# Kernel tuning notes

Hardware: AMD Instinct MI355X
Metric: run time of the kernel (lower is better)

Reference implementation:

```python
import jax, jax.numpy as jnp
import numpy as np

LN_EPS = 1e-5

def _reduce(t, ln_gamma, ln_beta, w_red, b_red):
    # LayerNorm(dim) then Linear(dim -> 16)
    mu = jnp.mean(t, axis=-1, keepdims=True)
    var = jnp.mean((t - mu) ** 2, axis=-1, keepdims=True)
    t = (t - mu) / jnp.sqrt(var + LN_EPS) * ln_gamma + ln_beta
    return t @ w_red + b_red  # [b, s, 16]

def setup_inputs() -> dict:
    key = jax.random.key(0)
    ks = jax.random.split(key, 4)
    b, m, n, dim, pair_dim = 1, 512, 512, 384, 128
    x = jax.random.normal(ks[0], (b, m, dim), dtype=jnp.float32)
    y = jax.random.normal(ks[1], (b, n, dim), dtype=jnp.float32)
    w_red = jax.random.normal(ks[2], (dim, 16), dtype=jnp.float32) / np.sqrt(dim)
    b_red = jnp.zeros((16,), dtype=jnp.float32)
    w_out = jax.random.normal(ks[3], (16 * 16, pair_dim), dtype=jnp.float32) / 16.0
    b_out = jnp.zeros((pair_dim,), dtype=jnp.float32)
    ln_gamma = jnp.ones((dim,), dtype=jnp.float32)
    ln_beta = jnp.zeros((dim,), dtype=jnp.float32)
    return {"x": x, "y": y, "ln_gamma": ln_gamma, "ln_beta": ln_beta,
            "w_red": w_red, "b_red": b_red, "w_out": w_out, "b_out": b_out}

def reference(x, y, ln_gamma, ln_beta, w_red, b_red, w_out, b_out):
    xr = _reduce(x, ln_gamma, ln_beta, w_red, b_red)  # [b, m, 16]
    yr = _reduce(y, ln_gamma, ln_beta, w_red, b_red)  # [b, n, 16]
    # outer product: [b, m, n, 16, 16]
    outer = jnp.einsum('bmi,bnj->bmnij', xr, yr)
    b_, m_, n_ = outer.shape[:3]
    outer = outer.reshape(b_, m_, n_, 16 * 16)
    return outer @ w_out + b_out  # [b, m, n, pair_dim]
```

## Files before the change

### kernel.cpp

```cpp
#include <hip/hip_runtime.h>

#define DIM 384
#define RD  16
#define PD  128
#define NN  512
#define LN_EPS 1e-5f

typedef float fx4 __attribute__((ext_vector_type(4)));

__global__ __launch_bounds__(128) void ln_reduce_kernel(
    const float* __restrict__ x, const float* __restrict__ y,
    const float* __restrict__ gamma, const float* __restrict__ beta,
    const float* __restrict__ w_red, const float* __restrict__ b_red,
    float* __restrict__ xr, float* __restrict__ yr, int M)
{
  int row = blockIdx.x;
  const float* src;
  float* dst;
  if (row < M) { src = x + (size_t)row * DIM;       dst = xr + (size_t)row * RD; }
  else         { src = y + (size_t)(row - M) * DIM; dst = yr + (size_t)(row - M) * RD; }

  int t = threadIdx.x;
  float v[3];
#pragma unroll
  for (int k = 0; k < 3; ++k) v[k] = src[t + k * 128];

  __shared__ float red[2];
  __shared__ float nrm[DIM];

  float s = v[0] + v[1] + v[2];
#pragma unroll
  for (int off = 32; off; off >>= 1) s += __shfl_down(s, off);
  int wave = t >> 6, lane = t & 63;
  if (lane == 0) red[wave] = s;
  __syncthreads();
  float mu = (red[0] + red[1]) * (1.0f / DIM);
  __syncthreads();

  float d0 = v[0] - mu, d1 = v[1] - mu, d2 = v[2] - mu;
  float s2 = d0 * d0 + d1 * d1 + d2 * d2;
#pragma unroll
  for (int off = 32; off; off >>= 1) s2 += __shfl_down(s2, off);
  if (lane == 0) red[wave] = s2;
  __syncthreads();
  float var = (red[0] + red[1]) * (1.0f / DIM);
  float rsig = rsqrtf(var + LN_EPS);

#pragma unroll
  for (int k = 0; k < 3; ++k) {
    int d = t + k * 128;
    nrm[d] = (v[k] - mu) * rsig * gamma[d] + beta[d];
  }
  __syncthreads();

  int j  = t >> 3;
  int k0 = t & 7;
  float p = 0.f;
  for (int e = k0; e < DIM; e += 8)
    p += nrm[e] * w_red[e * RD + j];
  p += __shfl_xor(p, 1);
  p += __shfl_xor(p, 2);
  p += __shfl_xor(p, 4);
  if (k0 == 0) dst[j] = p + b_red[j];
}

__global__ __launch_bounds__(512) void opm_kernel(
    const float* __restrict__ xr, const float* __restrict__ yr,
    const float* __restrict__ w_out, const float* __restrict__ b_out,
    float* __restrict__ out, int N)
{
  __shared__ float Vm[RD][PD];
  __shared__ float yrs[NN * RD];
  __shared__ float xm[RD];

  int m = blockIdx.x;
  int t = threadIdx.x;

  if (t < RD) xm[t] = xr[(size_t)m * RD + t];

  {
    fx4* d = (fx4*)yrs;
    const fx4* s4 = (const fx4*)yr;
    int total = N * RD / 4;
    for (int idx = t; idx < total; idx += 512) d[idx] = s4[idx];
  }
  __syncthreads();

  {
    int p  = t & 127;
    int j0 = (t >> 7) * 4;
#pragma unroll
    for (int jj = 0; jj < 4; ++jj) {
      int j = j0 + jj;
      float acc = 0.f;
#pragma unroll
      for (int i = 0; i < RD; ++i)
        acc += xm[i] * w_out[(size_t)(i * RD + j) * PD + p];
      Vm[j][p] = acc;
    }
  }
  __syncthreads();

  int p4 = (t & 31) * 4;
  int g  = t >> 5;

  fx4 w[RD];
#pragma unroll
  for (int j = 0; j < RD; ++j) w[j] = *(const fx4*)&Vm[j][p4];
  fx4 bo = *(const fx4*)&b_out[p4];

  float* obase = out + (size_t)m * N * PD + p4;

#pragma unroll 2
  for (int n = g; n < N; n += 16) {
    float yv[RD];
#pragma unroll
    for (int k = 0; k < 4; ++k)
      *(fx4*)&yv[k * 4] = *(const fx4*)&yrs[n * RD + k * 4];

    fx4 acc = bo;
#pragma unroll
    for (int j = 0; j < RD; ++j)
      acc += yv[j] * w[j];
    __builtin_nontemporal_store(acc, (fx4*)(obase + (size_t)n * PD));
  }
}

extern "C" void kernel_launch(void* const* d_in, const int* in_sizes, int n_in,
                              void* d_out, int out_size, void* d_ws, size_t ws_size,
                              hipStream_t stream) {
  const float* x        = (const float*)d_in[0];
  const float* y        = (const float*)d_in[1];
  const float* ln_gamma = (const float*)d_in[2];
  const float* ln_beta  = (const float*)d_in[3];
  const float* w_red    = (const float*)d_in[4];
  const float* b_red    = (const float*)d_in[5];
  const float* w_out    = (const float*)d_in[6];
  const float* b_out    = (const float*)d_in[7];
  float* out = (float*)d_out;

  int M = in_sizes[0] / DIM;
  int N = in_sizes[1] / DIM;

  float* xr = (float*)d_ws;
  float* yr = xr + (size_t)M * RD;

  ln_reduce_kernel<<<M + N, 128, 0, stream>>>(x, y, ln_gamma, ln_beta,
                                              w_red, b_red, xr, yr, M);

  opm_kernel<<<M, 512, 0, stream>>>(xr, yr, w_out, b_out, out, N);
}
```

Measured before the change: 44.76 us.

## Split OPM over n-chunks and precompute per-row Vm in separate kernel

The outer-product kernel now uses a 2D grid of n-chunks (128 columns) by m rows with 256 threads, instead of one 512-thread block per m that stages all of yr. When workspace allows, a new kernel first computes each row's 16x128 Vm matrix into global memory, and the main kernel loads it directly. Otherwise each block recomputes Vm locally. The output stores also switch from nontemporal to plain stores. This aims for more blocks and less shared memory per block, at the cost of an extra launch and Vm traffic or redundant Vm recomputation.

```diff
diff --git a/kernel.cpp b/kernel.cpp
--- a/kernel.cpp
+++ b/kernel.cpp
@@ -3,7 +3,7 @@
 #define DIM 384
 #define RD  16
 #define PD  128
-#define NN  512
+#define NCH 128
 #define LN_EPS 1e-5f
 
 typedef float fx4 __attribute__((ext_vector_type(4)));
@@ -64,65 +64,93 @@
   if (k0 == 0) dst[j] = p + b_red[j];
 }
 
-__global__ __launch_bounds__(512) void opm_kernel(
-    const float* __restrict__ xr, const float* __restrict__ yr,
+__global__ __launch_bounds__(256) void vm_kernel(
+    const float* __restrict__ xr, const float* __restrict__ w_out,
+    float* __restrict__ vm)
+{
+  int m = blockIdx.x;
+  int t = threadIdx.x;
+  __shared__ float xm[RD];
+  if (t < RD) xm[t] = xr[(size_t)m * RD + t];
+  __syncthreads();
+  int p  = t & 127;
+  int jh = t >> 7;
+#pragma unroll
+  for (int jj = 0; jj < 8; ++jj) {
+    int j = jh * 8 + jj;
+    float acc = 0.f;
+#pragma unroll
+    for (int i = 0; i < RD; ++i)
+      acc += xm[i] * w_out[(size_t)(i * RD + j) * PD + p];
+    vm[(size_t)m * RD * PD + j * PD + p] = acc;
+  }
+}
+
+template<int LOCAL>
+__global__ __launch_bounds__(256) void opm_kernel(
+    const float* __restrict__ vm_or_xr, const float* __restrict__ yr,
     const float* __restrict__ w_out, const float* __restrict__ b_out,
     float* __restrict__ out, int N)
 {
-  __shared__ float Vm[RD][PD];
-  __shared__ float yrs[NN * RD];
-  __shared__ float xm[RD];
+  __shared__ float ys[NCH * RD];
+  __shared__ float VmL[RD * PD];
 
-  int m = blockIdx.x;
-  int t = threadIdx.x;
-
-  if (t < RD) xm[t] = xr[(size_t)m * RD + t];
+  int m  = blockIdx.y;
+  int n0 = blockIdx.x * NCH;
+  int t  = threadIdx.x;
 
   {
-    fx4* d = (fx4*)yrs;
-    const fx4* s4 = (const fx4*)yr;
-    int total = N * RD / 4;
-    for (int idx = t; idx < total; idx += 512) d[idx] = s4[idx];
+    fx4* d = (fx4*)ys;
+    const fx4* s4 = (const fx4*)(yr + (size_t)n0 * RD);
+    d[t]       = s4[t];
+    d[t + 256] = s4[t + 256];
   }
-  __syncthreads();
 
-  {
+  int p4 = (t & 31) * 4;
+  int g  = t >> 5;
+  fx4 w[RD];
+
+  if (LOCAL) {
+    __shared__ float xm[RD];
+    if (t < RD) xm[t] = vm_or_xr[(size_t)m * RD + t];
+    __syncthreads();
     int p  = t & 127;
-    int j0 = (t >> 7) * 4;
+    int jh = t >> 7;
 #pragma unroll
-    for (int jj = 0; jj < 4; ++jj) {
-      int j = j0 + jj;
+    for (int jj = 0; jj < 8; ++jj) {
+      int j = jh * 8 + jj;
       float acc = 0.f;
 #pragma unroll
       for (int i = 0; i < RD; ++i)
         acc += xm[i] * w_out[(size_t)(i * RD + j) * PD + p];
-      Vm[j][p] = acc;
+      VmL[j * PD + p] = acc;
     }
+    __syncthreads();
+#pragma unroll
+    for (int j = 0; j < RD; ++j) w[j] = *(const fx4*)&VmL[j * PD + p4];
+  } else {
+    const float* vb = vm_or_xr + (size_t)m * RD * PD;
+#pragma unroll
+    for (int j = 0; j < RD; ++j) w[j] = *(const fx4*)&vb[j * PD + p4];
+    __syncthreads();
   }
-  __syncthreads();
 
-  int p4 = (t & 31) * 4;
-  int g  = t >> 5;
+  fx4 bo = *(const fx4*)&b_out[p4];
+  float* obase = out + ((size_t)m * N + n0) * PD + p4;
 
-  fx4 w[RD];
-#pragma unroll
-  for (int j = 0; j < RD; ++j) w[j] = *(const fx4*)&Vm[j][p4];
-  fx4 bo = *(const fx4*)&b_out[p4];
-
-  float* obase = out + (size_t)m * N * PD + p4;
-
-#pragma unroll 2
-  for (int n = g; n < N; n += 16) {
+#pragma unroll 4
+  for (int it = 0; it < NCH / 8; ++it) {
+    int n = it * 8 + g;
     float yv[RD];
 #pragma unroll
     for (int k = 0; k < 4; ++k)
-      *(fx4*)&yv[k * 4] = *(const fx4*)&yrs[n * RD + k * 4];
+      *(fx4*)&yv[k * 4] = *(const fx4*)&ys[n * RD + k * 4];
 
     fx4 acc = bo;
 #pragma unroll
     for (int j = 0; j < RD; ++j)
       acc += yv[j] * w[j];
-    __builtin_nontemporal_store(acc, (fx4*)(obase + (size_t)n * PD));
+    *(fx4*)(obase + (size_t)n * PD) = acc;
   }
 }
 
@@ -144,9 +172,18 @@
 
   float* xr = (float*)d_ws;
   float* yr = xr + (size_t)M * RD;
+  float* vm = yr + (size_t)N * RD;
+
+  size_t need = ((size_t)M * RD + (size_t)N * RD + (size_t)M * RD * PD) * 4;
 
   ln_reduce_kernel<<<M + N, 128, 0, stream>>>(x, y, ln_gamma, ln_beta,
                                               w_red, b_red, xr, yr, M);
 
-  opm_kernel<<<M, 512, 0, stream>>>(xr, yr, w_out, b_out, out, N);
+  dim3 grid(N / NCH, M);
+  if (ws_size >= need) {
+    vm_kernel<<<M, 256, 0, stream>>>(xr, w_out, vm);
+    opm_kernel<0><<<grid, 256, 0, stream>>>(vm, yr, w_out, b_out, out, N);
+  } else {
+    opm_kernel<1><<<grid, 256, 0, stream>>>(xr, yr, w_out, b_out, out, N);
+  }
 }
```

Result: slower. 54.61 us (+22.0%).
